# Performance work log

Measured on AMD Instinct MI355X. Metric: run time of the kernel, lower is better.

## Reference

```python
import jax, jax.numpy as jnp
import numpy as np

POS_DIM = 3
CAPACITY = 262144  # 2**18 hash-table slots per level
NR_LEVELS = 24
NR_FEAT = 2
N_POINTS = 524288
HASH_MUL = 2531011  # permutohedral-lattice hash multiplier (uint32 wraparound)


def _permuto_encode(positions, lattice_values, random_shift, anneal_window, scale_per_level):
    # positions: [N,d]  lattice_values: [L,C,F]  random_shift: [L,d]
    # anneal_window: [L]  scale_per_level: [L]
    N, d = positions.shape
    L, C, F = lattice_values.shape
    dp1 = d + 1
    dim = jnp.arange(d, dtype=positions.dtype)
    # per-level, per-axis scale: s_l / sqrt((i+1)(i+2))
    scale_factor = scale_per_level[:, None] / jnp.sqrt((dim + 1.0) * (dim + 2.0))  # [L,d]
    cf = (positions[None, :, :] + random_shift[:, None, :]) * scale_factor[:, None, :]  # [L,N,d]
    # elevate onto the hyperplane sum(x)=0 in R^{d+1}:
    # elevated[0]=sum(cf); elevated[i]=sum(cf[i:]) - i*cf[i-1]
    S = jnp.cumsum(cf[..., ::-1], axis=-1)[..., ::-1]            # suffix sums S[i]=sum cf[i:]
    S_next = jnp.concatenate([S[..., 1:], jnp.zeros_like(S[..., :1])], axis=-1)
    i_arr = jnp.arange(1, dp1, dtype=positions.dtype)
    elevated = jnp.concatenate([S[..., :1], S_next - i_arr * cf], axis=-1)  # [L,N,d+1]
    # nearest remainder-0 lattice point (round each coord to multiple of d+1)
    v = elevated / dp1
    up = jnp.ceil(v) * dp1
    down = jnp.floor(v) * dp1
    rem0 = jnp.where(up - elevated < elevated - down, up, down)  # [L,N,d+1]
    sum_val = jnp.round(jnp.sum(rem0, axis=-1) / dp1).astype(jnp.int32)  # [L,N]
    # rank: for i<j, if diff_i < diff_j then rank_i++ else rank_j++
    diff = elevated - rem0
    di = diff[..., :, None]
    dj = diff[..., None, :]
    ii = jnp.arange(dp1)[:, None]
    jj = jnp.arange(dp1)[None, :]
    rank = jnp.sum(jnp.where(jj > ii, dj > di, (jj < ii) & (dj >= di)), axis=-1).astype(jnp.int32)
    rank = rank + sum_val[..., None]
    under = rank < 0
    over = rank > d
    rank = rank + dp1 * under.astype(jnp.int32) - dp1 * over.astype(jnp.int32)
    rem0 = rem0 + dp1 * (under.astype(rem0.dtype) - over.astype(rem0.dtype))
    # barycentric weights: bary[d-rank_i] += delta_i; bary[d+1-rank_i] -= delta_i; bary[0] += 1 + bary[d+1]
    delta = (elevated - rem0) / dp1  # [L,N,d+1]
    t = d - rank
    bary = []
    for k in range(dp1 + 1):
        mk = (t == k).astype(delta.dtype) - (t == k - 1).astype(delta.dtype)
        bary.append(jnp.sum(delta * mk, axis=-1))  # [L,N]
    bary[0] = bary[0] + 1.0 + bary[dp1]
    # hash the d+1 simplex vertices; key[i] = rem0[i] + r - (d+1)*[rank[i] > d-r]
    rem0i = jnp.round(rem0).astype(jnp.int32)
    r = jnp.arange(dp1, dtype=jnp.int32)  # remainder axis -> simplex vertex
    h = jnp.zeros((L, N, dp1), dtype=jnp.uint32)
    for i in range(d):  # tiny structural loop over pos_dim
        key_i = rem0i[..., i:i + 1] + r - dp1 * (rank[..., i:i + 1] > d - r).astype(jnp.int32)
        h = (h + key_i.astype(jnp.uint32)) * jnp.uint32(HASH_MUL)
    ix = (h % jnp.uint32(C)).astype(jnp.int32)  # [L,N,d+1]
    # gather the d+1 vertex feature vectors per level and blend barycentrically
    gather = jax.vmap(lambda table, idx: table[idx])  # vmap over levels
    out = jnp.zeros((L, N, F), dtype=lattice_values.dtype)
    for rr in range(dp1):  # tiny structural loop over simplex vertices
        out = out + bary[rr][..., None] * gather(lattice_values, ix[..., rr])
    out = out * anneal_window[:, None, None]
    # kernel outputs [L,F,N] -> permute(2,0,1).reshape(N, L*F)
    return jnp.transpose(out, (1, 0, 2)).reshape(N, L * F)


def setup_inputs() -> dict:
    key = jax.random.key(0)
    k1, k2, k3 = jax.random.split(key, 3)
    positions = jax.random.uniform(k1, (N_POINTS, POS_DIM), dtype=jnp.float32)
    lattice_values = jax.random.normal(k2, (NR_LEVELS, CAPACITY, NR_FEAT), dtype=jnp.float32) * 1e-5
    random_shift = jax.random.normal(k3, (NR_LEVELS, POS_DIM), dtype=jnp.float32) * 10.0
    anneal_window = jnp.ones((NR_LEVELS,), dtype=jnp.float32)
    scale_per_level = jnp.asarray(np.geomspace(16.0, 2048.0, NR_LEVELS), dtype=jnp.float32)
    return {"positions": positions, "lattice_values": lattice_values,
            "random_shift": random_shift, "anneal_window": anneal_window,
            "scale_per_level": scale_per_level}


def reference(positions, lattice_values, random_shift, anneal_window, scale_per_level):
    return _permuto_encode(positions, lattice_values, random_shift, anneal_window, scale_per_level)
```

## Files before the change

kernel.cpp:

```cpp
#include <hip/hip_runtime.h>
#include <cstdint>

#define NPOINTS 524288
#define NLEV 24
#define CAP 262144
#define HASHMUL 2531011u
#define PTS_PER_BLOCK 512
#define BLOCKS_PER_LEVEL (NPOINTS / PTS_PER_BLOCK)

#define NBUCKET 4096
#define SORT_BLOCKS 64
#define SORT_PTS (NPOINTS / SORT_BLOCKS)

#define WS_H_B   ((size_t)NLEV * NPOINTS * 4)
#define POS4_B   ((size_t)NPOINTS * 16)
#define PART_B   ((size_t)SORT_BLOCKS * NBUCKET * 4)
#define BASE_B   PART_B
#define TOT_B    ((size_t)NBUCKET * 4)

typedef float v2f  __attribute__((ext_vector_type(2)));
typedef float v4f  __attribute__((ext_vector_type(4)));
typedef _Float16 f16x2 __attribute__((ext_vector_type(2)));


__device__ __forceinline__ uint32_t expand_bits(uint32_t v) {
    v = (v | (v << 16)) & 0x030000FFu;
    v = (v | (v << 8))  & 0x0300F00Fu;
    v = (v | (v << 4))  & 0x030C30C3u;
    v = (v | (v << 2))  & 0x09249249u;
    return v;
}

__device__ __forceinline__ uint32_t morton4(float x, float y, float z) {
    int xi = (int)(x * 16.0f); xi = xi < 0 ? 0 : (xi > 15 ? 15 : xi);
    int yi = (int)(y * 16.0f); yi = yi < 0 ? 0 : (yi > 15 ? 15 : yi);
    int zi = (int)(z * 16.0f); zi = zi < 0 ? 0 : (zi > 15 ? 15 : zi);
    return expand_bits((uint32_t)xi) | (expand_bits((uint32_t)yi) << 1)
         | (expand_bits((uint32_t)zi) << 2);
}

__global__ __launch_bounds__(256) void hist_kernel(
    const float* __restrict__ pos, int* __restrict__ part) {
    __shared__ int h[NBUCKET];
    const int t = threadIdx.x, b = blockIdx.x;
    #pragma unroll
    for (int i = t; i < NBUCKET; i += 256) h[i] = 0;
    __syncthreads();
    const int n0 = b * SORT_PTS;
    for (int i = 0; i < SORT_PTS / 256; ++i) {
        const int n = n0 + i * 256 + t;
        atomicAdd(&h[morton4(pos[n*3], pos[n*3+1], pos[n*3+2])], 1);
    }
    __syncthreads();
    #pragma unroll
    for (int i = t; i < NBUCKET; i += 256) part[b * NBUCKET + i] = h[i];
}

__global__ __launch_bounds__(256) void scanA_kernel(
    const int* __restrict__ part, int* __restrict__ tot) {
    const int j = blockIdx.x * 256 + threadIdx.x;
    int s = 0;
    #pragma unroll 8
    for (int b = 0; b < SORT_BLOCKS; ++b) s += part[b * NBUCKET + j];
    tot[j] = s;
}

__global__ __launch_bounds__(256) void scanB_kernel(
    const int* __restrict__ tot, int* __restrict__ G) {
    __shared__ int sums[256];
    const int t = threadIdx.x;
    const int CH = NBUCKET / 256;
    int loc[CH];
    int s = 0;
    #pragma unroll
    for (int k = 0; k < CH; ++k) { loc[k] = tot[t * CH + k]; s += loc[k]; }
    sums[t] = s;
    __syncthreads();
    for (int d = 1; d < 256; d <<= 1) {
        int v = (t >= d) ? sums[t - d] : 0;
        __syncthreads();
        sums[t] += v;
        __syncthreads();
    }
    int run = sums[t] - s;
    #pragma unroll
    for (int k = 0; k < CH; ++k) { G[t * CH + k] = run; run += loc[k]; }
}

__global__ __launch_bounds__(256) void scanC_kernel(
    const int* __restrict__ part, const int* __restrict__ G,
    int* __restrict__ base) {
    const int j = blockIdx.x * 256 + threadIdx.x;
    int run = G[j];
    #pragma unroll 8
    for (int b = 0; b < SORT_BLOCKS; ++b) {
        base[b * NBUCKET + j] = run;
        run += part[b * NBUCKET + j];
    }
}

__global__ __launch_bounds__(256) void scatter_kernel(
    const float* __restrict__ pos, const int* __restrict__ base,
    v4f* __restrict__ pos4) {
    __shared__ int cnt[NBUCKET];
    const int t = threadIdx.x, b = blockIdx.x;
    #pragma unroll
    for (int i = t; i < NBUCKET; i += 256) cnt[i] = base[b * NBUCKET + i];
    __syncthreads();
    const int n0 = b * SORT_PTS;
    for (int i = 0; i < SORT_PTS / 256; ++i) {
        const int n = n0 + i * 256 + t;
        const float x = pos[n*3], y = pos[n*3+1], z = pos[n*3+2];
        const int slot = atomicAdd(&cnt[morton4(x, y, z)], 1);
        v4f v; v.x = x; v.y = y; v.z = z; v.w = __uint_as_float((uint32_t)n);
        pos4[slot] = v;
    }
}


__device__ __forceinline__ void prep_point(
    const float p0, const float p1, const float p2,
    const float sf0, const float sf1, const float sf2,
    const float sh0, const float sh1, const float sh2,
    uint32_t* __restrict__ ix, float* __restrict__ w)
{
    const float cf0 = (p0 + sh0) * sf0;
    const float cf1 = (p1 + sh1) * sf1;
    const float cf2 = (p2 + sh2) * sf2;

    const float S2 = cf2;
    const float S1 = cf2 + cf1;
    const float S0 = S1 + cf0;

    float E[4];
    E[0] = S0;
    E[1] = S1 - 1.0f*cf0;
    E[2] = S2 - 2.0f*cf1;
    E[3] = 0.0f - 3.0f*cf2;

    float rem0[4];
    float sumrem = 0.0f;
    #pragma unroll
    for (int i = 0; i < 4; ++i) {
        float v  = E[i] * 0.25f;
        float up = ceilf(v)  * 4.0f;
        float dn = floorf(v) * 4.0f;
        rem0[i] = (up - E[i] < E[i] - dn) ? up : dn;
        sumrem += rem0[i];
    }
    const int sum_val = (int)rintf(sumrem * 0.25f);

    float diff[4];
    #pragma unroll
    for (int i = 0; i < 4; ++i) diff[i] = E[i] - rem0[i];

    int rank[4];
    #pragma unroll
    for (int i = 0; i < 4; ++i) {
        int rk = 0;
        #pragma unroll
        for (int j = 0; j < 4; ++j) {
            if (j > i)      rk += (diff[j] >  diff[i]) ? 1 : 0;
            else if (j < i) rk += (diff[j] >= diff[i]) ? 1 : 0;
        }
        rk += sum_val;
        if (rk < 0)      { rk += 4; rem0[i] += 4.0f; }
        else if (rk > 3) { rk -= 4; rem0[i] -= 4.0f; }
        rank[i] = rk;
    }

    float delta[4];
    #pragma unroll
    for (int i = 0; i < 4; ++i) delta[i] = (E[i] - rem0[i]) * 0.25f;

    float b[5];
    #pragma unroll
    for (int k = 0; k < 5; ++k) {
        float acc = 0.0f;
        #pragma unroll
        for (int i = 0; i < 4; ++i) {
            int ti = 3 - rank[i];
            float m = ((ti == k) ? 1.0f : 0.0f) - ((ti == (k-1)) ? 1.0f : 0.0f);
            acc += delta[i] * m;
        }
        b[k] = acc;
    }
    b[0] += 1.0f + b[4];

    int rem0i[4];
    #pragma unroll
    for (int i = 0; i < 4; ++i) rem0i[i] = (int)rintf(rem0[i]);

    #pragma unroll
    for (int r = 0; r < 4; ++r) {
        uint32_t h = 0u;
        #pragma unroll
        for (int i = 0; i < 3; ++i) {
            int key = rem0i[i] + r - 4 * ((rank[i] > 3 - r) ? 1 : 0);
            h = (h + (uint32_t)key) * HASHMUL;
        }
        ix[r] = h & (uint32_t)(CAP - 1);
        w[r]  = b[r];
    }
}

__device__ __forceinline__ uint32_t pack_h2_scaled(float x, float y) {
    f16x2 ph;
    ph.x = (_Float16)(x * 256.0f);
    ph.y = (_Float16)(y * 256.0f);
    return __builtin_bit_cast(uint32_t, ph);
}

__global__ __launch_bounds__(256, 6) void permuto_kernel(
    const v4f* __restrict__ pos4,
    const float* __restrict__ lattice,
    const float* __restrict__ shift,
    const float* __restrict__ anneal,
    const float* __restrict__ scale,
    uint32_t* __restrict__ ws_u)
{
    __shared__ v4f s_pos[PTS_PER_BLOCK];

    const int t    = threadIdx.x;
    const int bid  = blockIdx.x;
    const int xcd  = bid & 7;
    const int nb   = bid >> 3;
    const int pbase = nb * PTS_PER_BLOCK;

    {
        const v4f* src = pos4 + pbase;
        s_pos[t]       = src[t];
        s_pos[t + 256] = src[t + 256];
    }
    __syncthreads();

    const v4f pA = s_pos[t];
    const v4f pB = s_pos[t + 256];

    for (int ph = 0; ph < 3; ++ph) {
        const int l = xcd + 8 * ph;

        const float sc  = scale[l];
        const float sf0 = sc / sqrtf(2.0f);
        const float sf1 = sc / sqrtf(6.0f);
        const float sf2 = sc / sqrtf(12.0f);
        const float sh0 = shift[l*3+0];
        const float sh1 = shift[l*3+1];
        const float sh2 = shift[l*3+2];
        const float an  = anneal[l];

        uint32_t ixA[4], ixB[4];
        float    wA[4],  wB[4];
        prep_point(pA.x, pA.y, pA.z, sf0, sf1, sf2, sh0, sh1, sh2, ixA, wA);
        prep_point(pB.x, pB.y, pB.z, sf0, sf1, sf2, sh0, sh1, sh2, ixB, wB);

        const v2f* __restrict__ tbl =
            reinterpret_cast<const v2f*>(lattice) + (size_t)l * CAP;

        v2f vA[4], vB[4];
        #pragma unroll
        for (int r = 0; r < 4; ++r) vA[r] = tbl[ixA[r]];
        #pragma unroll
        for (int r = 0; r < 4; ++r) vB[r] = tbl[ixB[r]];

        float oA0 = 0.f, oA1 = 0.f, oB0 = 0.f, oB1 = 0.f;
        #pragma unroll
        for (int r = 0; r < 4; ++r) {
            oA0 += wA[r] * vA[r].x;  oA1 += wA[r] * vA[r].y;
            oB0 += wB[r] * vB[r].x;  oB1 += wB[r] * vB[r].y;
        }

        const uint32_t uA = pack_h2_scaled(oA0 * an, oA1 * an);
        const uint32_t uB = pack_h2_scaled(oB0 * an, oB1 * an);

        uint32_t* pWA = ws_u + (size_t)l * NPOINTS + pbase + t;
        __builtin_nontemporal_store(uA, pWA);
        __builtin_nontemporal_store(uB, pWA + 256);
    }
}

__global__ __launch_bounds__(256) void transpose_kernel(
    const uint32_t* __restrict__ ws_u,
    const uint32_t* __restrict__ pos4u,
    float* __restrict__ out)
{
    const int t  = threadIdx.x;
    const int m  = t & 3;
    const int p  = blockIdx.x * 64 + (t >> 2);

    const uint32_t orig = pos4u[4*p + 3];

    float r[12];
    #pragma unroll
    for (int i = 0; i < 6; ++i) {
        const int l = m * 6 + i;
        const uint32_t u = ws_u[(size_t)l * NPOINTS + p];
        const f16x2 hh = __builtin_bit_cast(f16x2, u);
        r[2*i+0] = (float)hh.x * 0.00390625f;
        r[2*i+1] = (float)hh.y * 0.00390625f;
    }

    float* orow = out + (size_t)orig * 48 + m * 12;
    #pragma unroll
    for (int j = 0; j < 3; ++j) {
        v4f v; v.x = r[4*j]; v.y = r[4*j+1]; v.z = r[4*j+2]; v.w = r[4*j+3];
        *reinterpret_cast<v4f*>(orow + 4*j) = v;
    }
}

__global__ __launch_bounds__(256) void permuto_direct(
    const float* __restrict__ pos,
    const float* __restrict__ lattice,
    const float* __restrict__ shift,
    const float* __restrict__ anneal,
    const float* __restrict__ scale,
    float* __restrict__ out)
{
    const int tid = blockIdx.x * 256 + threadIdx.x;
    const int n = tid / NLEV;
    const int l = tid - n * NLEV;

    const float sc  = scale[l];
    const float sf0 = sc / sqrtf(2.0f);
    const float sf1 = sc / sqrtf(6.0f);
    const float sf2 = sc / sqrtf(12.0f);

    uint32_t ix[4]; float w[4];
    prep_point(pos[n*3+0], pos[n*3+1], pos[n*3+2],
               sf0, sf1, sf2, shift[l*3+0], shift[l*3+1], shift[l*3+2], ix, w);

    const v2f* tbl = reinterpret_cast<const v2f*>(lattice) + (size_t)l * CAP;
    float o0 = 0.f, o1 = 0.f;
    #pragma unroll
    for (int r = 0; r < 4; ++r) {
        v2f v = tbl[ix[r]];
        o0 += w[r] * v.x;  o1 += w[r] * v.y;
    }
    const float an = anneal[l];
    v2f res; res.x = o0 * an; res.y = o1 * an;
    *reinterpret_cast<v2f*>(out + (size_t)n * (NLEV*2) + l*2) = res;
}

extern "C" void kernel_launch(void* const* d_in, const int* in_sizes, int n_in,
                              void* d_out, int out_size, void* d_ws, size_t ws_size,
                              hipStream_t stream) {
    const float* pos     = (const float*)d_in[0];
    const float* lattice = (const float*)d_in[1];
    const float* shift   = (const float*)d_in[2];
    const float* anneal  = (const float*)d_in[3];
    const float* scale   = (const float*)d_in[4];
    float* out = (float*)d_out;

    uint8_t* w8 = (uint8_t*)d_ws;
    uint32_t* ws_u  = (uint32_t*)w8;
    v4f*      pos4  = (v4f*)(w8 + WS_H_B);
    int*      part  = (int*)(w8 + WS_H_B + POS4_B);
    int*      basep = (int*)(w8 + WS_H_B + POS4_B + PART_B);
    int*      tot   = (int*)(w8 + WS_H_B + POS4_B + PART_B + BASE_B);
    int*      G     = (int*)(w8 + WS_H_B + POS4_B + PART_B + BASE_B + TOT_B);
    const size_t need = WS_H_B + POS4_B + PART_B + BASE_B + 2 * TOT_B;

    if (ws_size >= need) {
        hist_kernel   <<<SORT_BLOCKS, 256, 0, stream>>>(pos, part);
        scanA_kernel  <<<NBUCKET / 256, 256, 0, stream>>>(part, tot);
        scanB_kernel  <<<1, 256, 0, stream>>>(tot, G);
        scanC_kernel  <<<NBUCKET / 256, 256, 0, stream>>>(part, G, basep);
        scatter_kernel<<<SORT_BLOCKS, 256, 0, stream>>>(pos, basep, pos4);
        permuto_kernel<<<BLOCKS_PER_LEVEL * 8, 256, 0, stream>>>(
            pos4, lattice, shift, anneal, scale, ws_u);
        transpose_kernel<<<NPOINTS / 64, 256, 0, stream>>>(
            ws_u, (const uint32_t*)pos4, out);
    } else {
        permuto_direct<<<(NPOINTS * NLEV) / 256, 256, 0, stream>>>(
            pos, lattice, shift, anneal, scale, out);
    }
}
```

Measured before the change: 234.9 us.

## Fuse spatial-sort kernels into one cooperative kernel and refine buckets

Replaces the five sort kernels (histogram, three scan stages, scatter) with a single cooperative kernel that uses grid-wide syncs between phases. This removes four kernel launches and the gaps between them. It also raises the bucket count from 4096 to 16384 (32x32x16 grid) so the sorted points have finer spatial locality for the later lattice lookups. The cost is 64 KB of shared memory per block for the histogram, larger partial arrays to scan, and grid-sync overhead.

```diff
diff --git a/kernel.cpp b/kernel.cpp
--- a/kernel.cpp
+++ b/kernel.cpp
@@ -1,5 +1,8 @@
 #include <hip/hip_runtime.h>
+#include <hip/hip_cooperative_groups.h>
 #include <cstdint>
+
+namespace cg = cooperative_groups;
 
 #define NPOINTS 524288
 #define NLEV 24
@@ -8,7 +11,7 @@
 #define PTS_PER_BLOCK 512
 #define BLOCKS_PER_LEVEL (NPOINTS / PTS_PER_BLOCK)
 
-#define NBUCKET 4096
+#define NBUCKET 16384
 #define SORT_BLOCKS 64
 #define SORT_PTS (NPOINTS / SORT_BLOCKS)
 
@@ -16,7 +19,7 @@
 #define POS4_B   ((size_t)NPOINTS * 16)
 #define PART_B   ((size_t)SORT_BLOCKS * NBUCKET * 4)
 #define BASE_B   PART_B
-#define TOT_B    ((size_t)NBUCKET * 4)
+#define BT_B     ((size_t)4096)
 
 typedef float v2f  __attribute__((ext_vector_type(2)));
 typedef float v4f  __attribute__((ext_vector_type(4)));
@@ -31,87 +34,73 @@
     return v;
 }
 
-__device__ __forceinline__ uint32_t morton4(float x, float y, float z) {
-    int xi = (int)(x * 16.0f); xi = xi < 0 ? 0 : (xi > 15 ? 15 : xi);
-    int yi = (int)(y * 16.0f); yi = yi < 0 ? 0 : (yi > 15 ? 15 : yi);
+__device__ __forceinline__ uint32_t bucket_code(float x, float y, float z) {
+    int xi = (int)(x * 32.0f); xi = xi < 0 ? 0 : (xi > 31 ? 31 : xi);
+    int yi = (int)(y * 32.0f); yi = yi < 0 ? 0 : (yi > 31 ? 31 : yi);
     int zi = (int)(z * 16.0f); zi = zi < 0 ? 0 : (zi > 15 ? 15 : zi);
-    return expand_bits((uint32_t)xi) | (expand_bits((uint32_t)yi) << 1)
-         | (expand_bits((uint32_t)zi) << 2);
-}
-
-__global__ __launch_bounds__(256) void hist_kernel(
-    const float* __restrict__ pos, int* __restrict__ part) {
+    uint32_t m = expand_bits((uint32_t)(xi & 15))
+               | (expand_bits((uint32_t)(yi & 15)) << 1)
+               | (expand_bits((uint32_t)zi) << 2);
+    return m | ((uint32_t)(yi >> 4) << 12) | ((uint32_t)(xi >> 4) << 13);
+}
+
+__global__ __launch_bounds__(256) void sort_coop(
+    const float* __restrict__ pos,
+    int* __restrict__ part,
+    int* __restrict__ base,
+    int* __restrict__ blockTot,
+    v4f* __restrict__ pos4)
+{
+    cg::grid_group grid = cg::this_grid();
     __shared__ int h[NBUCKET];
     const int t = threadIdx.x, b = blockIdx.x;
-    #pragma unroll
+    const int n0 = b * SORT_PTS;
+
     for (int i = t; i < NBUCKET; i += 256) h[i] = 0;
     __syncthreads();
-    const int n0 = b * SORT_PTS;
     for (int i = 0; i < SORT_PTS / 256; ++i) {
         const int n = n0 + i * 256 + t;
-        atomicAdd(&h[morton4(pos[n*3], pos[n*3+1], pos[n*3+2])], 1);
-    }
-    __syncthreads();
-    #pragma unroll
+        atomicAdd(&h[bucket_code(pos[n*3], pos[n*3+1], pos[n*3+2])], 1);
+    }
+    __syncthreads();
     for (int i = t; i < NBUCKET; i += 256) part[b * NBUCKET + i] = h[i];
-}
-
-__global__ __launch_bounds__(256) void scanA_kernel(
-    const int* __restrict__ part, int* __restrict__ tot) {
-    const int j = blockIdx.x * 256 + threadIdx.x;
-    int s = 0;
+    grid.sync();
+
+    const int j = b * 256 + t;
+    int tot = 0;
     #pragma unroll 8
-    for (int b = 0; b < SORT_BLOCKS; ++b) s += part[b * NBUCKET + j];
-    tot[j] = s;
-}
-
-__global__ __launch_bounds__(256) void scanB_kernel(
-    const int* __restrict__ tot, int* __restrict__ G) {
-    __shared__ int sums[256];
-    const int t = threadIdx.x;
-    const int CH = NBUCKET / 256;
-    int loc[CH];
-    int s = 0;
-    #pragma unroll
-    for (int k = 0; k < CH; ++k) { loc[k] = tot[t * CH + k]; s += loc[k]; }
-    sums[t] = s;
+    for (int bb = 0; bb < SORT_BLOCKS; ++bb) tot += part[bb * NBUCKET + j];
+    __syncthreads();
+    h[t] = tot;
     __syncthreads();
     for (int d = 1; d < 256; d <<= 1) {
-        int v = (t >= d) ? sums[t - d] : 0;
+        int v = (t >= d) ? h[t - d] : 0;
         __syncthreads();
-        sums[t] += v;
+        h[t] += v;
         __syncthreads();
     }
-    int run = sums[t] - s;
-    #pragma unroll
-    for (int k = 0; k < CH; ++k) { G[t * CH + k] = run; run += loc[k]; }
-}
-
-__global__ __launch_bounds__(256) void scanC_kernel(
-    const int* __restrict__ part, const int* __restrict__ G,
-    int* __restrict__ base) {
-    const int j = blockIdx.x * 256 + threadIdx.x;
-    int run = G[j];
+    const int excl = h[t] - tot;
+    if (t == 255) blockTot[b] = h[255];
+    grid.sync();
+
+    if (t < SORT_BLOCKS) h[256 + t] = blockTot[t];
+    __syncthreads();
+    int G0 = 0;
+    for (int i = 0; i < b; ++i) G0 += h[256 + i];
+    int run = G0 + excl;
     #pragma unroll 8
-    for (int b = 0; b < SORT_BLOCKS; ++b) {
-        base[b * NBUCKET + j] = run;
-        run += part[b * NBUCKET + j];
-    }
-}
-
-__global__ __launch_bounds__(256) void scatter_kernel(
-    const float* __restrict__ pos, const int* __restrict__ base,
-    v4f* __restrict__ pos4) {
-    __shared__ int cnt[NBUCKET];
-    const int t = threadIdx.x, b = blockIdx.x;
-    #pragma unroll
-    for (int i = t; i < NBUCKET; i += 256) cnt[i] = base[b * NBUCKET + i];
-    __syncthreads();
-    const int n0 = b * SORT_PTS;
+    for (int bb = 0; bb < SORT_BLOCKS; ++bb) {
+        base[bb * NBUCKET + j] = run;
+        run += part[bb * NBUCKET + j];
+    }
+    grid.sync();
+
+    for (int i = t; i < NBUCKET; i += 256) h[i] = base[b * NBUCKET + i];
+    __syncthreads();
     for (int i = 0; i < SORT_PTS / 256; ++i) {
         const int n = n0 + i * 256 + t;
         const float x = pos[n*3], y = pos[n*3+1], z = pos[n*3+2];
-        const int slot = atomicAdd(&cnt[morton4(x, y, z)], 1);
+        const int slot = atomicAdd(&h[bucket_code(x, y, z)], 1);
         v4f v; v.x = x; v.y = y; v.z = z; v.w = __uint_as_float((uint32_t)n);
         pos4[slot] = v;
     }
@@ -356,16 +345,14 @@
     v4f*      pos4  = (v4f*)(w8 + WS_H_B);
     int*      part  = (int*)(w8 + WS_H_B + POS4_B);
     int*      basep = (int*)(w8 + WS_H_B + POS4_B + PART_B);
-    int*      tot   = (int*)(w8 + WS_H_B + POS4_B + PART_B + BASE_B);
-    int*      G     = (int*)(w8 + WS_H_B + POS4_B + PART_B + BASE_B + TOT_B);
-    const size_t need = WS_H_B + POS4_B + PART_B + BASE_B + 2 * TOT_B;
+    int*      btot  = (int*)(w8 + WS_H_B + POS4_B + PART_B + BASE_B);
+    const size_t need = WS_H_B + POS4_B + PART_B + BASE_B + BT_B;
 
     if (ws_size >= need) {
-        hist_kernel   <<<SORT_BLOCKS, 256, 0, stream>>>(pos, part);
-        scanA_kernel  <<<NBUCKET / 256, 256, 0, stream>>>(part, tot);
-        scanB_kernel  <<<1, 256, 0, stream>>>(tot, G);
-        scanC_kernel  <<<NBUCKET / 256, 256, 0, stream>>>(part, G, basep);
-        scatter_kernel<<<SORT_BLOCKS, 256, 0, stream>>>(pos, basep, pos4);
+        void* args[] = { (void*)&pos, (void*)&part, (void*)&basep,
+                         (void*)&btot, (void*)&pos4 };
+        hipLaunchCooperativeKernel(reinterpret_cast<void*>(sort_coop),
+                                   dim3(SORT_BLOCKS), dim3(256), args, 0, stream);
         permuto_kernel<<<BLOCKS_PER_LEVEL * 8, 256, 0, stream>>>(
             pos4, lattice, shift, anneal, scale, ws_u);
         transpose_kernel<<<NPOINTS / 64, 256, 0, stream>>>(
```

Measured after the change: 277.5 us. +18.1%, slower.
